# Kernel tuning notes

Measured on AMD Instinct MI355X. Metric: run time of the kernel, lower is better.

## Reference

```python
import jax, jax.numpy as jnp
import numpy as np

DIM = 1024
HEAD_DIM = 64
NUM_HEADS = DIM // HEAD_DIM
SCALE = HEAD_DIM ** -0.5
B, N, M = 2, 1024, 2048


def setup_inputs() -> dict:
    key = jax.random.key(0)
    ks = jax.random.split(key, 7)
    x = jax.random.normal(ks[0], (B, N, DIM), dtype=jnp.float32)
    context = jax.random.normal(ks[1], (B, M, DIM), dtype=jnp.float32)
    # query row has at least one valid key (avoids all -inf softmax rows).
    mask = jax.random.bernoulli(ks[2], 0.9, (B, N, M))
    mask = mask.at[:, :, 0].set(True)
    # Linear params (torch nn.Linear convention: y = x @ W.T + b)
    sq = (1.0 / DIM) ** 0.5
    Wq = jax.random.uniform(ks[3], (DIM, DIM), minval=-sq, maxval=sq, dtype=jnp.float32)
    Wkv = jax.random.uniform(ks[4], (2 * DIM, DIM), minval=-sq, maxval=sq, dtype=jnp.float32)
    b_kv = jax.random.uniform(ks[5], (2 * DIM,), minval=-sq, maxval=sq, dtype=jnp.float32)
    Wo = jax.random.uniform(ks[6], (DIM, DIM), minval=-sq, maxval=sq, dtype=jnp.float32)
    return {"x": x, "context": context, "mask": mask,
            "Wq": Wq, "Wkv": Wkv, "b_kv": b_kv, "Wo": Wo}


def reference(x, context, mask, Wq, Wkv, b_kv, Wo):
    b, n, c = x.shape
    m = context.shape[1]
    h, d = NUM_HEADS, HEAD_DIM
    # Q projection (no bias): [b, n, h, d] -> bhnd
    q = (x @ Wq.T).reshape(b, n, h, d).transpose(0, 2, 1, 3)
    # KV projection (with bias): [b, m, 2, h, d]
    kv = (context @ Wkv.T + b_kv).reshape(b, m, 2, h, d)
    k = kv[:, :, 0].transpose(0, 2, 1, 3)  # bhmd
    v = kv[:, :, 1].transpose(0, 2, 1, 3)  # bhmd
    # scores: bhnm, scale applied after matmul as in the original
    attn = jnp.einsum('bhnd,bhmd->bhnm', q, k) * SCALE
    attn = jnp.where(mask[:, None, :, :], attn, -jnp.inf)
    attn = jax.nn.softmax(attn, axis=-1)
    out = jnp.einsum('bhnm,bhmd->bhnd', attn, v)
    out = out.transpose(0, 2, 1, 3).reshape(b, n, h * d)
    return out @ Wo.T
```

## Files before the change

### kernel.cpp

```cpp
#include <hip/hip_runtime.h>


typedef __attribute__((ext_vector_type(8))) short short8;
typedef __attribute__((ext_vector_type(4))) short short4v;
typedef __attribute__((ext_vector_type(4))) float f32x4;
typedef __attribute__((ext_vector_type(4))) int int4v;

#define SCL2E 0.18033688011112042592f

__device__ __forceinline__ float bf2f(short s) {
  unsigned u = ((unsigned)(unsigned short)s) << 16;
  return __uint_as_float(u);
}
__device__ __forceinline__ short f2bf(float f) {
  unsigned u = __float_as_uint(f);
  u += 0x7fffu + ((u >> 16) & 1u);
  return (short)(u >> 16);
}
__device__ __forceinline__ int cvt_pk_bf16(float a, float b) {
  int r;
  asm("v_cvt_pk_bf16_f32 %0, %1, %2" : "=v"(r) : "v"(a), "v"(b));
  return r;
}
__device__ __forceinline__ void gld_lds16(const void* gp, void* lp) {
  __builtin_amdgcn_global_load_lds(
      (const __attribute__((address_space(1))) unsigned int*)gp,
      (__attribute__((address_space(3))) unsigned int*)lp, 16, 0, 0);
}
__device__ __forceinline__ void sbar() {
  __builtin_amdgcn_sched_barrier(0);
  __builtin_amdgcn_s_barrier();
  __builtin_amdgcn_sched_barrier(0);
}
#define WAITVM(N) asm volatile("s_waitcnt vmcnt(" #N ")" ::: "memory")

__device__ __forceinline__ void pipesync() {
  asm volatile("s_waitcnt vmcnt(0) lgkmcnt(0)" ::: "memory");
  __builtin_amdgcn_sched_barrier(0);
  __builtin_amdgcn_s_barrier();
  __builtin_amdgcn_sched_barrier(0);
}
__device__ __forceinline__ short4v cvt4(float4 v) {
  short4v o;
  o[0] = f2bf(v.x); o[1] = f2bf(v.y); o[2] = f2bf(v.z); o[3] = f2bf(v.w);
  return o;
}
__device__ __forceinline__ size_t off128(int row, int k) {
  return ((size_t)(((row >> 7) * 32 + (k >> 5)) * 8 + ((row >> 4) & 7)) << 9) +
         (((((k >> 3) & 3) * 16 + (row & 15)) << 3) + (k & 7));
}
__device__ __forceinline__ size_t off64(int row, int k) {
  return ((size_t)(((row >> 6) * 32 + (k >> 5)) * 4 + ((row >> 4) & 3)) << 9) +
         (((((k >> 3) & 3) * 16 + (row & 15)) << 3) + (k & 7));
}

__global__ __launch_bounds__(256) void prep(
    const unsigned char* __restrict__ mask, unsigned long long* __restrict__ pm,
    const float* __restrict__ Wq, const float* __restrict__ Wkv,
    const float* __restrict__ Wo, const float* __restrict__ x,
    const float* __restrict__ ctx, short* __restrict__ wqb,
    short* __restrict__ wkvb, short* __restrict__ wob,
    short* __restrict__ xb, short* __restrict__ ctxb) {
  const int row = blockIdx.x;
  const int wave = threadIdx.x >> 6, lane = threadIdx.x & 63;
  const unsigned char p8 = mask[lane * 4 + 1];
  const int p32 = ((const int*)mask)[lane * 2 + 1];
  const int shift =
      (__ballot(p8 != 0) != 0ull) ? 0 : ((__ballot(p32 != 0) != 0ull) ? 2 : 3);
  const size_t mbase = ((size_t)row * 2048) << shift;
#pragma unroll
  for (int j = 0; j < 8; j++) {
    const int c = wave * 512 + j * 64 + lane;
    const unsigned long long bits = __ballot(mask[mbase + ((size_t)c << shift)] != 0);
    if (lane == 0) pm[(size_t)row * 32 + wave * 8 + j] = bits;
  }
  const int gid = blockIdx.x * 256 + threadIdx.x;
  {
    const int e = gid * 4, r = e >> 10, k = e & 1023;
    *(short4v*)(xb + off128(r, k)) = cvt4(((const float4*)x)[gid]);
  }
  {
    int e = gid * 4, r = e >> 10, k = e & 1023;
    *(short4v*)(ctxb + off128(r, k)) = cvt4(((const float4*)ctx)[gid]);
    e = (gid + 524288) * 4; r = e >> 10; k = e & 1023;
    *(short4v*)(ctxb + off128(r, k)) = cvt4(((const float4*)ctx)[gid + 524288]);
  }
  {
    const int e = gid * 4, r = e >> 10, k = e & 1023;
    *(short4v*)(wkvb + off128(r, k)) = cvt4(((const float4*)Wkv)[gid]);
  }
  if (gid < 262144) {
    const int e = gid * 4, r = e >> 10, k = e & 1023;
    *(short4v*)(wqb + off128(r, k)) = cvt4(((const float4*)Wq)[gid]);
    *(short4v*)(wob + off64(r, k)) = cvt4(((const float4*)Wo)[gid]);
  }
}

__global__ __launch_bounds__(256, 3)
void qkv_gemm(const short* __restrict__ xb, const short* __restrict__ ctxb,
              const short* __restrict__ wqb, const short* __restrict__ wkvb,
              const float* __restrict__ bias, short* __restrict__ qws,
              short* __restrict__ kws, short* __restrict__ vtws) {
  __shared__ __align__(16) short ldsA[3][4096];
  __shared__ __align__(16) short ldsB[3][4096];
  const int tid = threadIdx.x;
  const int wave = tid >> 6, lane = tid & 63;
  const int l15 = lane & 15, lg = lane >> 4;
  const int bx0 = blockIdx.x;
  const int bx = (bx0 & 7) * 80 + (bx0 >> 3);
  const bool isKV = bx < 512;
  const int rt = isKV ? (bx >> 4) : ((bx - 512) >> 3);
  const int ct = isKV ? (bx & 15) : ((bx - 512) & 7);
  const short* Amat = isKV ? ctxb : xb;
  const short* Bw = isKV ? wkvb : wqb;
  const int wr = wave >> 1, wc = wave & 1;

  f32x4 acc[4][4];
#pragma unroll
  for (int i = 0; i < 4; i++)
#pragma unroll
    for (int j = 0; j < 4; j++) acc[i][j] = (f32x4){0.f, 0.f, 0.f, 0.f};

  const short* ga0 = Amat + (size_t)rt * 131072 + wave * 512 + lane * 8;
  const short* ga1 = ga0 + 2048;
  const short* gb0 = Bw + (size_t)ct * 131072 + wave * 512 + lane * 8;
  const short* gb1 = gb0 + 2048;

  auto stage = [&](int kk, int buf) {
    const size_t koff = (size_t)kk * 4096;
    short* dA = &ldsA[buf][0];
    short* dB = &ldsB[buf][0];
    gld_lds16(ga0 + koff, dA + wave * 512);
    gld_lds16(ga1 + koff, dA + (wave + 4) * 512);
    gld_lds16(gb0 + koff, dB + wave * 512);
    gld_lds16(gb1 + koff, dB + (wave + 4) * 512);
  };
  auto compute = [&](int buf) {
    const short* sA = &ldsA[buf][0];
    const short* sB = &ldsB[buf][0];
    short8 af[4], bfr[4];
#pragma unroll
    for (int t = 0; t < 4; t++)
      af[t] = *(const short8*)&sA[((wr * 4 + t) * 64 + lane) * 8];
#pragma unroll
    for (int t = 0; t < 4; t++)
      bfr[t] = *(const short8*)&sB[((wc * 4 + t) * 64 + lane) * 8];
#pragma unroll
    for (int i = 0; i < 4; i++)
#pragma unroll
      for (int j = 0; j < 4; j++)
        acc[i][j] =
            __builtin_amdgcn_mfma_f32_16x16x32_bf16(af[i], bfr[j], acc[i][j], 0, 0, 0);
  };

  stage(0, 0);
  stage(1, 1);
  int cur = 0, nxt = 2;
  for (int i = 0; i < 30; ++i) {
    WAITVM(4);
    sbar();
    stage(i + 2, nxt);
    compute(cur);
    cur = (cur == 2) ? 0 : cur + 1;
    nxt = (nxt == 2) ? 0 : nxt + 1;
  }
  WAITVM(4);
  sbar();
  compute(cur);
  cur = (cur == 2) ? 0 : cur + 1;
  WAITVM(0);
  sbar();
  compute(cur);

#pragma unroll
  for (int i = 0; i < 4; i++)
#pragma unroll
    for (int j = 0; j < 4; j++)
#pragma unroll
      for (int r = 0; r < 4; r++) {
        const int gr = rt * 128 + wr * 64 + i * 16 + lg * 4 + r;
        const int gc = ct * 128 + wc * 64 + j * 16 + l15;
        float v = acc[i][j][r];
        if (isKV) {
          v += bias[gc];
          const int b = gr >> 11, m = gr & 2047;
          const int kv = gc >> 10, hh = (gc >> 6) & 15, d = gc & 63;
          if (kv == 0)
            kws[((((size_t)b * 16 + hh) * 2048 + m) << 6) + d] = f2bf(v);
          else {
            const int mp = (m & ~31) | (((m >> 2) & 3) << 3) |
                           (((m >> 4) & 1) << 2) | (m & 3);
            vtws[(((size_t)b * 16 + hh) * 64 + d) * 2048 + mp] = f2bf(v);
          }
        } else {
          const int b = gr >> 10, n = gr & 1023, hh = gc >> 6, d = gc & 63;
          qws[((((size_t)b * 16 + hh) * 1024 + n) << 6) + d] = f2bf(v * SCL2E);
        }
      }
}

__global__ __launch_bounds__(512, 4)
void attn_split(const short* __restrict__ Qg, const short* __restrict__ Kg,
                const short* __restrict__ Vtg,
                const unsigned int* __restrict__ pm,
                float* __restrict__ opart, float* __restrict__ lpart) {
  __shared__ __align__(16) short ldsK[2][8192];
  __shared__ __align__(16) short ldsV[2][8192];
  const int tid = threadIdx.x;
  const int w = tid >> 6, lane = tid & 63;
  const int l15 = lane & 15, lg = lane >> 4;
  const int bx = blockIdx.x;
  const int bhid = bx & 31, qt = (bx >> 5) & 7, half = bx >> 8;
  const int b = bhid >> 4, h = bhid & 15;
  const int n0 = qt * 128, m_base = half * 1024;
  const size_t bh = (size_t)b * 16 + h;
  const short* Qb = Qg + (bh * 1024 + n0) * 64;
  const short* Kb = Kg + (bh << 17);
  const short* Vb = Vtg + (bh << 17);
  const unsigned int* pmw =
      pm + ((size_t)(b * 1024 + n0 + w * 16 + l15) << 6) + (m_base >> 5);

  uint4 mku[8];
#pragma unroll
  for (int c = 0; c < 8; c++) mku[c] = *(const uint4*)(pmw + c * 4);

  auto stageKV = [&](int c, int buf) {
    const int m0 = m_base + c * 128;
    short* dK = &ldsK[buf][0];
    short* dV = &ldsV[buf][0];
#pragma unroll
    for (int ii = 0; ii < 2; ii++) {
      const int f = w * 2 + ii;
      const int t = f >> 1, ks = f & 1;
      gld_lds16(Kb + (size_t)(m0 + t * 16 + l15) * 64 + ks * 32 + lg * 8,
                dK + f * 512);
      const int vt = f >> 2, vk = f & 3;
      gld_lds16(Vb + (size_t)(vt * 16 + l15) * 2048 + (m0 + vk * 32 + lg * 8),
                dV + f * 512);
    }
  };

#pragma unroll
  for (int ii = 0; ii < 2; ii++)
    gld_lds16(Qb + (size_t)(w * 16 + l15) * 64 + ii * 32 + lg * 8,
              &ldsV[1][(w * 2 + ii) * 512]);
  stageKV(0, 0);
  pipesync();
  short8 qf[2];
#pragma unroll
  for (int ks = 0; ks < 2; ks++)
    qf[ks] = *(const short8*)&ldsV[1][((w * 2 + ks) * 64 + lane) * 8];
  asm volatile("s_waitcnt lgkmcnt(0)" ::: "memory");
  sbar();

  short8 onesf;
#pragma unroll
  for (int i = 0; i < 8; i++) onesf[i] = (short)0x3F80;

  f32x4 o[4], lacc;
#pragma unroll
  for (int ct = 0; ct < 4; ct++) o[ct] = (f32x4){0.f, 0.f, 0.f, 0.f};
  lacc = (f32x4){0.f, 0.f, 0.f, 0.f};
  const int sb = lg * 4;

  auto computeC = [&](uint4 mk, int buf) {
    const short* sK = &ldsK[buf][0];
    const short* sV = &ldsV[buf][0];
    int4v pw4[4];
#pragma unroll
    for (int h2 = 0; h2 < 2; h2++) {
      f32x4 s[4];
#pragma unroll
      for (int t2 = 0; t2 < 4; t2++) s[t2] = (f32x4){0.f, 0.f, 0.f, 0.f};
#pragma unroll
      for (int t2 = 0; t2 < 4; t2++) {
        const int t = h2 * 4 + t2;
#pragma unroll
        for (int ks = 0; ks < 2; ks++) {
          const short8 kf = *(const short8*)&sK[((t * 2 + ks) * 64 + lane) * 8];
          s[t2] = __builtin_amdgcn_mfma_f32_16x16x32_bf16(kf, qf[ks], s[t2], 0, 0, 0);
        }
      }
#pragma unroll
      for (int t2 = 0; t2 < 4; t2++) {
        const int t = h2 * 4 + t2;
        const unsigned int mw = ((t >> 1) == 0) ? mk.x
                              : ((t >> 1) == 1) ? mk.y
                              : ((t >> 1) == 2) ? mk.z : mk.w;
        float p[4];
#pragma unroll
        for (int r = 0; r < 4; r++) {
          const bool att = (mw >> (((t & 1) << 4) + sb + r)) & 1;
          p[r] = exp2f(att ? s[t2][r] : -1e30f);
        }
        pw4[t >> 1][(t & 1) * 2] = cvt_pk_bf16(p[0], p[1]);
        pw4[t >> 1][(t & 1) * 2 + 1] = cvt_pk_bf16(p[2], p[3]);
      }
    }
#pragma unroll
    for (int ks2 = 0; ks2 < 4; ks2++) {
      const short8 pf = __builtin_bit_cast(short8, pw4[ks2]);
#pragma unroll
      for (int ct = 0; ct < 4; ct++) {
        const short8 vf = *(const short8*)&sV[((ct * 4 + ks2) * 64 + lane) * 8];
        o[ct] = __builtin_amdgcn_mfma_f32_16x16x32_bf16(pf, vf, o[ct], 0, 0, 0);
      }
      lacc = __builtin_amdgcn_mfma_f32_16x16x32_bf16(pf, onesf, lacc, 0, 0, 0);
    }
  };

#pragma unroll
  for (int c = 0; c < 8; c++) {
    if (c + 1 < 8) {
      stageKV(c + 1, (c + 1) & 1);
      WAITVM(4);
    } else {
      WAITVM(0);
    }
    sbar();
    computeC(mku[c], c & 1);
    sbar();
  }

#pragma unroll
  for (int ct = 0; ct < 4; ct++)
#pragma unroll
    for (int r = 0; r < 4; r++) {
      const int n = n0 + w * 16 + lg * 4 + r;
      opart[((size_t)half << 21) + (((size_t)b * 1024 + n) << 10) + h * 64 +
            ct * 16 + l15] = o[ct][r];
    }
  if (l15 == 0) {
#pragma unroll
    for (int r = 0; r < 4; r++) {
      const int n = n0 + w * 16 + lg * 4 + r;
      lpart[((size_t)half << 15) + bh * 1024 + n] = lacc[r];
    }
  }
}

__global__ __launch_bounds__(256) void combine(
    const float* __restrict__ opart, const float* __restrict__ lpart,
    short* __restrict__ aoT) {
  const int gid = blockIdx.x * 256 + threadIdx.x;
  const size_t base = (size_t)gid * 4;
  const int row = (int)(base >> 10), col = (int)(base & 1023);
  const int b = row >> 10, n = row & 1023, h = col >> 6;
  const float4 o1 = *(const float4*)(opart + base);
  const float4 o2 = *(const float4*)(opart + (1u << 21) + base);
  const float l1 = lpart[(size_t)(b * 16 + h) * 1024 + n];
  const float l2 = lpart[(1u << 15) + (size_t)(b * 16 + h) * 1024 + n];
  const float inv = 1.f / fmaxf(l1 + l2, 1e-30f);
  short4v o;
  o[0] = f2bf((o1.x + o2.x) * inv); o[1] = f2bf((o1.y + o2.y) * inv);
  o[2] = f2bf((o1.z + o2.z) * inv); o[3] = f2bf((o1.w + o2.w) * inv);
  *(short4v*)(aoT + off64(row, col)) = o;
}

__global__ __launch_bounds__(256, 3)
void o_gemm(const short* __restrict__ aoT, const short* __restrict__ wobT,
            float* __restrict__ Of) {
  __shared__ __align__(16) short ldsA[3][4096];
  __shared__ __align__(16) short ldsB[3][4096];
  const int tid = threadIdx.x;
  const int w = tid >> 6, lane = tid & 63;
  const int l15 = lane & 15, lg = lane >> 4;
  const int bx0 = blockIdx.x;
  const int bx = (bx0 & 7) * 64 + (bx0 >> 3);
  const int rt = bx >> 4, ct = bx & 15;

  f32x4 acc[4];
#pragma unroll
  for (int j = 0; j < 4; j++) acc[j] = (f32x4){0.f, 0.f, 0.f, 0.f};

  const short* ga = aoT + (size_t)rt * 65536 + w * 512 + lane * 8;
  const short* gb = wobT + (size_t)ct * 65536 + w * 512 + lane * 8;

  auto stage = [&](int t, int buf) {
    const size_t koff = (size_t)t * 4096;
    gld_lds16(ga + koff, &ldsA[buf][0] + w * 512);
    gld_lds16(ga + koff + 2048, &ldsA[buf][0] + 2048 + w * 512);
    gld_lds16(gb + koff, &ldsB[buf][0] + w * 512);
    gld_lds16(gb + koff + 2048, &ldsB[buf][0] + 2048 + w * 512);
  };
  auto compute = [&](int buf) {
    const short* sA = &ldsA[buf][0];
    const short* sB = &ldsB[buf][0];
    const short8 af0 = *(const short8*)&sA[(w * 64 + lane) * 8];
    const short8 af1 = *(const short8*)&sA[2048 + (w * 64 + lane) * 8];
#pragma unroll
    for (int j = 0; j < 4; j++) {
      const short8 bf0 = *(const short8*)&sB[(j * 64 + lane) * 8];
      const short8 bf1 = *(const short8*)&sB[2048 + (j * 64 + lane) * 8];
      acc[j] = __builtin_amdgcn_mfma_f32_16x16x32_bf16(af0, bf0, acc[j], 0, 0, 0);
      acc[j] = __builtin_amdgcn_mfma_f32_16x16x32_bf16(af1, bf1, acc[j], 0, 0, 0);
    }
  };

  stage(0, 0);
  stage(1, 1);
#pragma unroll
  for (int i = 0; i < 14; ++i) {
    WAITVM(4);
    sbar();
    stage(i + 2, (i + 2) % 3);
    compute(i % 3);
  }
  WAITVM(4);
  sbar();
  compute(14 % 3);
  WAITVM(0);
  sbar();
  compute(15 % 3);

#pragma unroll
  for (int j = 0; j < 4; j++)
#pragma unroll
    for (int r = 0; r < 4; r++) {
      const int gr = rt * 64 + w * 16 + lg * 4 + r;
      const int gc = ct * 64 + j * 16 + l15;
      Of[(size_t)gr * 1024 + gc] = acc[j][r];
    }
}

extern "C" void kernel_launch(void* const* d_in, const int* in_sizes, int n_in,
                              void* d_out, int out_size, void* d_ws, size_t ws_size,
                              hipStream_t stream) {
  const float* x   = (const float*)d_in[0];
  const float* ctx = (const float*)d_in[1];
  const unsigned char* mask = (const unsigned char*)d_in[2];
  const float* Wq  = (const float*)d_in[3];
  const float* Wkv = (const float*)d_in[4];
  const float* bkv = (const float*)d_in[5];
  const float* Wo  = (const float*)d_in[6];
  float* out = (float*)d_out;

  char* wsb = (char*)d_ws;
  short* qws  = (short*)(wsb);
  short* kws  = (short*)(wsb + (4u << 20));
  short* vtws = (short*)(wsb + (12u << 20));
  short* wqb  = (short*)(wsb + (20u << 20));
  short* wkvb = (short*)(wsb + (22u << 20));
  short* wob  = (short*)(wsb + (26u << 20));
  unsigned long long* pmws = (unsigned long long*)(wsb + (28u << 20));
  float* opart = (float*)(wsb + (29u << 20));
  float* lpart = (float*)(wsb + (45u << 20));
  short* xb   = (short*)(wsb + (29u << 20));
  short* ctxb = (short*)(wsb + (33u << 20));
  short* ao = (short*)(wsb + (20u << 20));

  prep<<<2048, 256, 0, stream>>>(mask, pmws, Wq, Wkv, Wo, x, ctx,
                                 wqb, wkvb, wob, xb, ctxb);
  qkv_gemm<<<640, 256, 0, stream>>>(xb, ctxb, wqb, wkvb, bkv, qws, kws, vtws);
  attn_split<<<512, 512, 0, stream>>>(qws, kws, vtws, (const unsigned int*)pmws,
                                      opart, lpart);
  combine<<<2048, 256, 0, stream>>>(opart, lpart, ao);
  o_gemm<<<512, 256, 0, stream>>>(ao, wob, out);
}
```

Before: 221.8 us.

## Process two query tiles per wave in attention to reuse K/V fragments

The attention kernel now runs 256 threads per block instead of 512. Each wave handles 32 query rows as two 16-row tiles, so every K and V fragment read from LDS feeds two MFMAs. Staging loads per thread double to cover the same 128-key chunk, and mask words are now loaded per chunk inside the loop instead of being preloaded into registers. The aim is to halve LDS reads per MFMA and expose more independent MFMA chains per wave. In exchange, register pressure per wave rises and there are half as many waves per block to hide latency.

```diff
diff --git a/kernel.cpp b/kernel.cpp
--- a/kernel.cpp
+++ b/kernel.cpp
@@ -199,7 +199,7 @@
       }
 }
 
-__global__ __launch_bounds__(512, 4)
+__global__ __launch_bounds__(256, 2)
 void attn_split(const short* __restrict__ Qg, const short* __restrict__ Kg,
                 const short* __restrict__ Vtg,
                 const unsigned int* __restrict__ pm,
@@ -217,20 +217,17 @@
   const short* Qb = Qg + (bh * 1024 + n0) * 64;
   const short* Kb = Kg + (bh << 17);
   const short* Vb = Vtg + (bh << 17);
-  const unsigned int* pmw =
-      pm + ((size_t)(b * 1024 + n0 + w * 16 + l15) << 6) + (m_base >> 5);
-
-  uint4 mku[8];
-#pragma unroll
-  for (int c = 0; c < 8; c++) mku[c] = *(const uint4*)(pmw + c * 4);
+  const unsigned int* pmwA =
+      pm + ((size_t)(b * 1024 + n0 + w * 32 + l15) << 6) + (m_base >> 5);
+  const unsigned int* pmwB = pmwA + (16 << 6);
 
   auto stageKV = [&](int c, int buf) {
     const int m0 = m_base + c * 128;
     short* dK = &ldsK[buf][0];
     short* dV = &ldsV[buf][0];
 #pragma unroll
-    for (int ii = 0; ii < 2; ii++) {
-      const int f = w * 2 + ii;
+    for (int ii = 0; ii < 4; ii++) {
+      const int f = w * 4 + ii;
       const int t = f >> 1, ks = f & 1;
       gld_lds16(Kb + (size_t)(m0 + t * 16 + l15) * 64 + ks * 32 + lg * 8,
                 dK + f * 512);
@@ -241,15 +238,20 @@
   };
 
 #pragma unroll
-  for (int ii = 0; ii < 2; ii++)
-    gld_lds16(Qb + (size_t)(w * 16 + l15) * 64 + ii * 32 + lg * 8,
-              &ldsV[1][(w * 2 + ii) * 512]);
+  for (int ii = 0; ii < 4; ii++) {
+    const int f = w * 4 + ii;
+    const int t = f >> 1, ks = f & 1;
+    gld_lds16(Qb + (size_t)(t * 16 + l15) * 64 + ks * 32 + lg * 8,
+              &ldsV[1][f * 512]);
+  }
   stageKV(0, 0);
   pipesync();
-  short8 qf[2];
-#pragma unroll
-  for (int ks = 0; ks < 2; ks++)
-    qf[ks] = *(const short8*)&ldsV[1][((w * 2 + ks) * 64 + lane) * 8];
+  short8 qfA[2], qfB[2];
+#pragma unroll
+  for (int ks = 0; ks < 2; ks++) {
+    qfA[ks] = *(const short8*)&ldsV[1][(((w * 2 + 0) * 2 + ks) * 64 + lane) * 8];
+    qfB[ks] = *(const short8*)&ldsV[1][(((w * 2 + 1) * 2 + ks) * 64 + lane) * 8];
+  }
   asm volatile("s_waitcnt lgkmcnt(0)" ::: "memory");
   sbar();
 
@@ -257,68 +259,87 @@
 #pragma unroll
   for (int i = 0; i < 8; i++) onesf[i] = (short)0x3F80;
 
-  f32x4 o[4], lacc;
-#pragma unroll
-  for (int ct = 0; ct < 4; ct++) o[ct] = (f32x4){0.f, 0.f, 0.f, 0.f};
-  lacc = (f32x4){0.f, 0.f, 0.f, 0.f};
+  f32x4 oA[4], oB[4], laccA, laccB;
+#pragma unroll
+  for (int ct = 0; ct < 4; ct++) {
+    oA[ct] = (f32x4){0.f, 0.f, 0.f, 0.f};
+    oB[ct] = (f32x4){0.f, 0.f, 0.f, 0.f};
+  }
+  laccA = (f32x4){0.f, 0.f, 0.f, 0.f};
+  laccB = (f32x4){0.f, 0.f, 0.f, 0.f};
   const int sb = lg * 4;
 
-  auto computeC = [&](uint4 mk, int buf) {
+  auto computeC = [&](uint4 mkA, uint4 mkB, int buf) {
     const short* sK = &ldsK[buf][0];
     const short* sV = &ldsV[buf][0];
-    int4v pw4[4];
+    int4v pwA[4], pwB[4];
 #pragma unroll
     for (int h2 = 0; h2 < 2; h2++) {
-      f32x4 s[4];
-#pragma unroll
-      for (int t2 = 0; t2 < 4; t2++) s[t2] = (f32x4){0.f, 0.f, 0.f, 0.f};
+      f32x4 sA[4], sB[4];
+#pragma unroll
+      for (int t2 = 0; t2 < 4; t2++) {
+        sA[t2] = (f32x4){0.f, 0.f, 0.f, 0.f};
+        sB[t2] = (f32x4){0.f, 0.f, 0.f, 0.f};
+      }
 #pragma unroll
       for (int t2 = 0; t2 < 4; t2++) {
         const int t = h2 * 4 + t2;
 #pragma unroll
         for (int ks = 0; ks < 2; ks++) {
           const short8 kf = *(const short8*)&sK[((t * 2 + ks) * 64 + lane) * 8];
-          s[t2] = __builtin_amdgcn_mfma_f32_16x16x32_bf16(kf, qf[ks], s[t2], 0, 0, 0);
+          sA[t2] = __builtin_amdgcn_mfma_f32_16x16x32_bf16(kf, qfA[ks], sA[t2], 0, 0, 0);
+          sB[t2] = __builtin_amdgcn_mfma_f32_16x16x32_bf16(kf, qfB[ks], sB[t2], 0, 0, 0);
         }
       }
 #pragma unroll
       for (int t2 = 0; t2 < 4; t2++) {
         const int t = h2 * 4 + t2;
-        const unsigned int mw = ((t >> 1) == 0) ? mk.x
-                              : ((t >> 1) == 1) ? mk.y
-                              : ((t >> 1) == 2) ? mk.z : mk.w;
-        float p[4];
+        const unsigned int mwA = ((t >> 1) == 0) ? mkA.x
+                               : ((t >> 1) == 1) ? mkA.y
+                               : ((t >> 1) == 2) ? mkA.z : mkA.w;
+        const unsigned int mwB = ((t >> 1) == 0) ? mkB.x
+                               : ((t >> 1) == 1) ? mkB.y
+                               : ((t >> 1) == 2) ? mkB.z : mkB.w;
+        float pA[4], pB[4];
 #pragma unroll
         for (int r = 0; r < 4; r++) {
-          const bool att = (mw >> (((t & 1) << 4) + sb + r)) & 1;
-          p[r] = exp2f(att ? s[t2][r] : -1e30f);
+          const int bit = ((t & 1) << 4) + sb + r;
+          pA[r] = exp2f(((mwA >> bit) & 1) ? sA[t2][r] : -1e30f);
+          pB[r] = exp2f(((mwB >> bit) & 1) ? sB[t2][r] : -1e30f);
         }
-        pw4[t >> 1][(t & 1) * 2] = cvt_pk_bf16(p[0], p[1]);
-        pw4[t >> 1][(t & 1) * 2 + 1] = cvt_pk_bf16(p[2], p[3]);
+        pwA[t >> 1][(t & 1) * 2] = cvt_pk_bf16(pA[0], pA[1]);
+        pwA[t >> 1][(t & 1) * 2 + 1] = cvt_pk_bf16(pA[2], pA[3]);
+        pwB[t >> 1][(t & 1) * 2] = cvt_pk_bf16(pB[0], pB[1]);
+        pwB[t >> 1][(t & 1) * 2 + 1] = cvt_pk_bf16(pB[2], pB[3]);
       }
     }
 #pragma unroll
     for (int ks2 = 0; ks2 < 4; ks2++) {
-      const short8 pf = __builtin_bit_cast(short8, pw4[ks2]);
+      const short8 pfA = __builtin_bit_cast(short8, pwA[ks2]);
+      const short8 pfB = __builtin_bit_cast(short8, pwB[ks2]);
 #pragma unroll
       for (int ct = 0; ct < 4; ct++) {
         const short8 vf = *(const short8*)&sV[((ct * 4 + ks2) * 64 + lane) * 8];
-        o[ct] = __builtin_amdgcn_mfma_f32_16x16x32_bf16(pf, vf, o[ct], 0, 0, 0);
+        oA[ct] = __builtin_amdgcn_mfma_f32_16x16x32_bf16(pfA, vf, oA[ct], 0, 0, 0);
+        oB[ct] = __builtin_amdgcn_mfma_f32_16x16x32_bf16(pfB, vf, oB[ct], 0, 0, 0);
       }
-      lacc = __builtin_amdgcn_mfma_f32_16x16x32_bf16(pf, onesf, lacc, 0, 0, 0);
+      laccA = __builtin_amdgcn_mfma_f32_16x16x32_bf16(pfA, onesf, laccA, 0, 0, 0);
+      laccB = __builtin_amdgcn_mfma_f32_16x16x32_bf16(pfB, onesf, laccB, 0, 0, 0);
     }
   };
 
 #pragma unroll
   for (int c = 0; c < 8; c++) {
+    const uint4 mkA = *(const uint4*)(pmwA + c * 4);
+    const uint4 mkB = *(const uint4*)(pmwB + c * 4);
     if (c + 1 < 8) {
       stageKV(c + 1, (c + 1) & 1);
-      WAITVM(4);
+      WAITVM(8);
     } else {
       WAITVM(0);
     }
     sbar();
-    computeC(mku[c], c & 1);
+    computeC(mkA, mkB, c & 1);
     sbar();
   }
 
@@ -326,15 +347,19 @@
   for (int ct = 0; ct < 4; ct++)
 #pragma unroll
     for (int r = 0; r < 4; r++) {
-      const int n = n0 + w * 16 + lg * 4 + r;
-      opart[((size_t)half << 21) + (((size_t)b * 1024 + n) << 10) + h * 64 +
-            ct * 16 + l15] = o[ct][r];
+      const int nA = n0 + w * 32 + lg * 4 + r;
+      const int nB = nA + 16;
+      opart[((size_t)half << 21) + (((size_t)b * 1024 + nA) << 10) + h * 64 +
+            ct * 16 + l15] = oA[ct][r];
+      opart[((size_t)half << 21) + (((size_t)b * 1024 + nB) << 10) + h * 64 +
+            ct * 16 + l15] = oB[ct][r];
     }
   if (l15 == 0) {
 #pragma unroll
     for (int r = 0; r < 4; r++) {
-      const int n = n0 + w * 16 + lg * 4 + r;
-      lpart[((size_t)half << 15) + bh * 1024 + n] = lacc[r];
+      const int nA = n0 + w * 32 + lg * 4 + r;
+      lpart[((size_t)half << 15) + bh * 1024 + nA] = laccA[r];
+      lpart[((size_t)half << 15) + bh * 1024 + nA + 16] = laccB[r];
     }
   }
 }
@@ -452,7 +477,7 @@
   prep<<<2048, 256, 0, stream>>>(mask, pmws, Wq, Wkv, Wo, x, ctx,
                                  wqb, wkvb, wob, xb, ctxb);
   qkv_gemm<<<640, 256, 0, stream>>>(xb, ctxb, wqb, wkvb, bkv, qws, kws, vtws);
-  attn_split<<<512, 512, 0, stream>>>(qws, kws, vtws, (const unsigned int*)pmws,
+  attn_split<<<512, 256, 0, stream>>>(qws, kws, vtws, (const unsigned int*)pmws,
                                       opart, lpart);
   combine<<<2048, 256, 0, stream>>>(opart, lpart, ao);
   o_gemm<<<512, 256, 0, stream>>>(ao, wob, out);
```

Result: slower. 226.3 us (+2.0%).

## Load QKV GEMM fragments directly from global into registers, drop LDS staging

Applied to the files above, without the earlier changes.

Replaces the LDS triple-buffered global-to-LDS staging with direct per-wave global loads of the pre-swizzled fragments into registers, double-buffered across k-steps. This removes the barriers and LDS traffic. In exchange each wave loads its own A/B fragments, so the data shared between waves in a block is fetched from global/L2 twice, and register pressure rises under launch bounds of 3 blocks per SM.

```diff
diff --git a/kernel.cpp b/kernel.cpp
--- a/kernel.cpp
+++ b/kernel.cpp
@@ -101,8 +101,6 @@
               const short* __restrict__ wqb, const short* __restrict__ wkvb,
               const float* __restrict__ bias, short* __restrict__ qws,
               short* __restrict__ kws, short* __restrict__ vtws) {
-  __shared__ __align__(16) short ldsA[3][4096];
-  __shared__ __align__(16) short ldsB[3][4096];
   const int tid = threadIdx.x;
   const int wave = tid >> 6, lane = tid & 63;
   const int l15 = lane & 15, lg = lane >> 4;
@@ -121,56 +119,35 @@
 #pragma unroll
     for (int j = 0; j < 4; j++) acc[i][j] = (f32x4){0.f, 0.f, 0.f, 0.f};
 
-  const short* ga0 = Amat + (size_t)rt * 131072 + wave * 512 + lane * 8;
-  const short* ga1 = ga0 + 2048;
-  const short* gb0 = Bw + (size_t)ct * 131072 + wave * 512 + lane * 8;
-  const short* gb1 = gb0 + 2048;
-
-  auto stage = [&](int kk, int buf) {
-    const size_t koff = (size_t)kk * 4096;
-    short* dA = &ldsA[buf][0];
-    short* dB = &ldsB[buf][0];
-    gld_lds16(ga0 + koff, dA + wave * 512);
-    gld_lds16(ga1 + koff, dA + (wave + 4) * 512);
-    gld_lds16(gb0 + koff, dB + wave * 512);
-    gld_lds16(gb1 + koff, dB + (wave + 4) * 512);
-  };
-  auto compute = [&](int buf) {
-    const short* sA = &ldsA[buf][0];
-    const short* sB = &ldsB[buf][0];
-    short8 af[4], bfr[4];
-#pragma unroll
-    for (int t = 0; t < 4; t++)
-      af[t] = *(const short8*)&sA[((wr * 4 + t) * 64 + lane) * 8];
-#pragma unroll
-    for (int t = 0; t < 4; t++)
-      bfr[t] = *(const short8*)&sB[((wc * 4 + t) * 64 + lane) * 8];
+  const short* pa = Amat + (size_t)rt * 131072 + (size_t)(wr * 4) * 512 + lane * 8;
+  const short* pb = Bw + (size_t)ct * 131072 + (size_t)(wc * 4) * 512 + lane * 8;
+
+  short8 aC[4], bC[4], aN[4], bN[4];
+  auto loadfr = [&](short8* da, short8* db, int kk) {
+    const size_t ko = (size_t)kk * 4096;
+#pragma unroll
+    for (int t = 0; t < 4; t++) {
+      da[t] = *(const short8*)(pa + ko + t * 512);
+      db[t] = *(const short8*)(pb + ko + t * 512);
+    }
+  };
+  auto mfmaall = [&](const short8* a, const short8* b) {
 #pragma unroll
     for (int i = 0; i < 4; i++)
 #pragma unroll
       for (int j = 0; j < 4; j++)
         acc[i][j] =
-            __builtin_amdgcn_mfma_f32_16x16x32_bf16(af[i], bfr[j], acc[i][j], 0, 0, 0);
-  };
-
-  stage(0, 0);
-  stage(1, 1);
-  int cur = 0, nxt = 2;
-  for (int i = 0; i < 30; ++i) {
-    WAITVM(4);
-    sbar();
-    stage(i + 2, nxt);
-    compute(cur);
-    cur = (cur == 2) ? 0 : cur + 1;
-    nxt = (nxt == 2) ? 0 : nxt + 1;
-  }
-  WAITVM(4);
-  sbar();
-  compute(cur);
-  cur = (cur == 2) ? 0 : cur + 1;
-  WAITVM(0);
-  sbar();
-  compute(cur);
+            __builtin_amdgcn_mfma_f32_16x16x32_bf16(a[i], b[j], acc[i][j], 0, 0, 0);
+  };
+
+  loadfr(aC, bC, 0);
+#pragma unroll
+  for (int kk = 0; kk < 32; kk += 2) {
+    loadfr(aN, bN, kk + 1);
+    mfmaall(aC, bC);
+    if (kk + 2 < 32) loadfr(aC, bC, kk + 2);
+    mfmaall(aN, bN);
+  }
 
 #pragma unroll
   for (int i = 0; i < 4; i++)
```

Measured after the change: 224.9 us. Within noise of the previous version (+1.4%).
